# Performance work log

Hardware: AMD Instinct MI355X
Metric: run time of the kernel (lower is better)

## Reference

```python
import jax, jax.numpy as jnp
import numpy as np

GROUP_SIZE = 128

def setup_inputs() -> dict:
    key = jax.random.key(0)
    k0, k1, k2, k3 = jax.random.split(key, 4)
    B, S, K, N = 4, 16, 8192, 28672
    G = GROUP_SIZE
    x = jax.random.normal(k0, (B, S, K), dtype=jnp.float16)
    # packed uint8 stored as int32 (2 int4 nibbles per byte along K)
    w_packed = jax.random.randint(k1, (K // 2, N), 0, 256, dtype=jnp.int32)
    # per-group positive scales, typical magnitude for int4 quant of fp16 weights
    scales = (jax.random.uniform(k2, (K // G, N), dtype=jnp.float32) * 0.02 + 1e-4).astype(jnp.float16)
    bias = (jax.random.normal(k3, (N,), dtype=jnp.float16) * 0.02).astype(jnp.float16)
    return {"x": x, "w_packed": w_packed, "scales": scales, "bias": bias}

def _dequant(w_packed, scales):
    # w_packed: [K//2, N] ints in [0,256); low nibble -> even k, high nibble -> odd k
    low = (w_packed & 15) - 8          # [K//2, N] int32 in [-8, 7]
    high = ((w_packed >> 4) & 15) - 8  # [K//2, N]
    Kh, N = w_packed.shape
    w_int = jnp.stack([low, high], axis=1).reshape(Kh * 2, N)  # interleave -> [K, N]
    s = jnp.repeat(scales, GROUP_SIZE, axis=0)                 # [K, N] fp16
    return w_int.astype(jnp.float16) * s                       # [K, N] fp16

def reference(x, w_packed, scales, bias):
    # x: [B, S, K] fp16 -> y: [B, S, N] fp16
    w = _dequant(w_packed, scales)                 # [K, N] fp16
    lead = x.shape[:-1]
    x2 = x.reshape(-1, x.shape[-1])                # [M, K]
    # fp32 accumulation, fp16 output (matches Triton kernel's tl.dot accumulator)
    y = jnp.dot(x2, w, preferred_element_type=jnp.float32).astype(jnp.float16)
    y = y + bias
    return y.reshape(*lead, -1)
```

## Files before the change

### kernel.cpp

```cpp
#include <hip/hip_runtime.h>


typedef short  short8  __attribute__((ext_vector_type(8)));
typedef float  float4v __attribute__((ext_vector_type(4)));
typedef int    int4v   __attribute__((ext_vector_type(4)));
typedef unsigned int uint4v __attribute__((ext_vector_type(4)));

constexpr int Kd = 8192;
constexpr int Nd = 28672;
constexpr int KSPLIT = 4;

__device__ __forceinline__ unsigned f32_to_bf16_rn(float f) {
    unsigned u = __builtin_bit_cast(unsigned, f);
    return (u + 0x7FFFu + ((u >> 16) & 1u)) >> 16;
}

__device__ __forceinline__ void async16(const void* g, void* l) {
    __builtin_amdgcn_global_load_lds(
        (const __attribute__((address_space(1))) unsigned*)g,
        (__attribute__((address_space(3))) unsigned*)l, 16, 0, 0);
}

__global__ __launch_bounds__(256)
void init_y_kernel(const float* __restrict__ bias, float* __restrict__ y) {
    const int gid = blockIdx.x * 256 + threadIdx.x;
    const int m  = gid / (Nd / 4);
    const int nq = gid % (Nd / 4);
    ((float4v*)y)[(long)m * (Nd / 4) + nq] = ((const float4v*)bias)[nq];
}

__global__ __launch_bounds__(256)
void cvt_x_kernel(const float* __restrict__ x, unsigned short* __restrict__ o) {
    const int i = (blockIdx.x * 256 + threadIdx.x) * 8;
    float4v a = *(const float4v*)(x + i);
    float4v b = *(const float4v*)(x + i + 4);
    union { unsigned short s[8]; short8 v; } r;
    #pragma unroll
    for (int j = 0; j < 4; ++j) {
        r.s[j]     = (unsigned short)f32_to_bf16_rn(a[j]);
        r.s[4 + j] = (unsigned short)f32_to_bf16_rn(b[j]);
    }
    *(short8*)(o + i) = r.v;
}

__global__ __launch_bounds__(256, 3)
void int4_main_kernel(const unsigned short* __restrict__ xw,
                      const int*            __restrict__ wp,
                      const float*          __restrict__ scales,
                      float*                __restrict__ y)
{
    __shared__ unsigned wbA[2048], wbB[2048], wbC[2048];
    __shared__ unsigned xbA[2048], xbB[2048], xbC[2048];
    __shared__ unsigned sb[1024];

    const int t = threadIdx.x, lane = t & 63, wv = t >> 6;
    const int q = lane >> 4, c = lane & 15;
    const int l4 = lane >> 4, l15 = lane & 15;
    const int n0 = blockIdx.x * 64, kz = blockIdx.y;

    const int* wsrc0; const int* wsrc1;
    {
        int r0 = wv * 8 + 0 * 4 + l4, c0 = (l15 * 4) ^ (((wv * 2 + 0) & 3) << 4);
        int r1 = wv * 8 + 1 * 4 + l4, c1 = (l15 * 4) ^ (((wv * 2 + 1) & 3) << 4);
        wsrc0 = wp + (long)(kz * 1024 + r0) * Nd + n0 + c0;
        wsrc1 = wp + (long)(kz * 1024 + r1) * Nd + n0 + c1;
    }
    const unsigned short* xsrc0; const unsigned short* xsrc1;
    {
        int s0 = wv * 128 + 0 * 64 + lane, m0 = s0 >> 3, k0 = (s0 & 7) ^ (m0 & 7);
        int s1 = wv * 128 + 1 * 64 + lane, m1 = s1 >> 3, k1 = (s1 & 7) ^ (m1 & 7);
        xsrc0 = xw + (long)m0 * Kd + kz * 2048 + k0 * 8;
        xsrc1 = xw + (long)m1 * Kd + kz * 2048 + k1 * 8;
    }
    const int ldof = wv * 512;

    auto stage = [&](int hg, unsigned* wbuf, unsigned* xbuf) {
        const long wof = (long)hg * 32 * Nd;
        const long xof = (long)hg * 64;
        async16(wsrc0 + wof, wbuf + ldof);
        async16(wsrc1 + wof, wbuf + ldof + 256);
        async16(xsrc0 + xof, xbuf + ldof);
        async16(xsrc1 + xof, xbuf + ldof + 256);
    };

    {
        const float* ssrc = scales + (long)(kz * 16 + (t >> 4)) * Nd + n0 + (t & 15) * 4;
        async16(ssrc, sb + wv * 256);
    }
    stage(0, wbA, xbA);
    stage(1, wbB, xbB);

    float4v acc[4] = {};

    auto compute = [&](const unsigned* wbuf, const unsigned* xbuf, int g) {
        const float s   = __builtin_bit_cast(float, sb[g * 64 + wv * 16 + c]);
        const float m8s = -8.0f * s;
        #pragma unroll
        for (int it = 0; it < 2; ++it) {
            union { short8 h; unsigned u[4]; } bu;
            #pragma unroll
            for (int i = 0; i < 4; ++i) {
                unsigned v = wbuf[(it * 16 + q * 4 + i) * 64 + ((wv * 16 + c) ^ (q << 4))];
                float lo = fmaf((float)(v & 15u), s, m8s);
                float hi = fmaf((float)((v >> 4) & 15u), s, m8s);
                bu.u[i] = f32_to_bf16_rn(lo) | (f32_to_bf16_rn(hi) << 16);
            }
            __builtin_amdgcn_s_setprio(1);
            #pragma unroll
            for (int mt = 0; mt < 4; ++mt) {
                int m = mt * 16 + c;
                int slot = m * 8 + ((it * 4 + q) ^ (c & 7));
                short8 a = *(const short8*)(xbuf + slot * 4);
                acc[mt] = __builtin_amdgcn_mfma_f32_16x16x32_bf16(a, bu.h, acc[mt], 0, 0, 0);
            }
            __builtin_amdgcn_s_setprio(0);
        }
    };

    for (int g3 = 0; g3 < 10; ++g3) {
        const int ph = 3 * g3;
        stage(ph + 2, wbC, xbC);
        asm volatile("s_waitcnt vmcnt(8)\ns_barrier" ::: "memory");
        compute(wbA, xbA, ph >> 1);
        asm volatile("s_waitcnt lgkmcnt(0)\ns_barrier" ::: "memory");
        stage(ph + 3, wbA, xbA);
        asm volatile("s_waitcnt vmcnt(8)\ns_barrier" ::: "memory");
        compute(wbB, xbB, (ph + 1) >> 1);
        asm volatile("s_waitcnt lgkmcnt(0)\ns_barrier" ::: "memory");
        stage(ph + 4, wbB, xbB);
        asm volatile("s_waitcnt vmcnt(8)\ns_barrier" ::: "memory");
        compute(wbC, xbC, (ph + 2) >> 1);
        asm volatile("s_waitcnt lgkmcnt(0)\ns_barrier" ::: "memory");
    }
    asm volatile("s_waitcnt vmcnt(4)\ns_barrier" ::: "memory");
    compute(wbA, xbA, 15);
    asm volatile("s_waitcnt lgkmcnt(0)\ns_barrier" ::: "memory");
    asm volatile("s_waitcnt vmcnt(0)\ns_barrier" ::: "memory");
    compute(wbB, xbB, 15);

    const int nw = n0 + wv * 16 + c;
    #pragma unroll
    for (int mt = 0; mt < 4; ++mt)
        #pragma unroll
        for (int r = 0; r < 4; ++r)
            atomicAdd(&y[(long)(mt * 16 + q * 4 + r) * Nd + nw], acc[mt][r]);
}

__global__ __launch_bounds__(256, 6)
void int4_main_nows_kernel(const float* __restrict__ xf,
                           const int*   __restrict__ wp,
                           const float* __restrict__ scales,
                           float*       __restrict__ y)
{
    constexpr int LDS_STRIDE = 68;
    __shared__ unsigned lds_w[64 * LDS_STRIDE];
    const int t = threadIdx.x, lane = t & 63, wv = t >> 6;
    const int q = lane >> 4, c = lane & 15;
    const int n0 = blockIdx.x * 64, kz = blockIdx.y;
    const int sr = t >> 4, ss = t & 15;
    const int*   wp_b = wp + (long)(kz * 1024 + sr) * Nd + n0 + 4 * ss;
    const float* sc_b = scales + (long)(kz * 16) * Nd + n0 + 4 * ss;
    const float* xf_b = xf + (long)c * Kd + kz * 2048 + q * 8;
    float4v acc[4] = {};

    for (int g = 0; g < 16; ++g) {
        const float4v s4 = *(const float4v*)(sc_b + (long)g * Nd);
        const int* wg = wp_b + (long)g * 64 * Nd;
        #pragma unroll
        for (int i = 0; i < 4; ++i) {
            int4v v = *(const int4v*)(wg + (long)i * 16 * Nd);
            uint4v pk;
            #pragma unroll
            for (int j = 0; j < 4; ++j) {
                float lo = (float)((v[j] & 15) - 8) * s4[j];
                float hi = (float)(((v[j] >> 4) & 15) - 8) * s4[j];
                pk[j] = f32_to_bf16_rn(lo) | (f32_to_bf16_rn(hi) << 16);
            }
            *(uint4v*)&lds_w[(i * 16 + sr) * LDS_STRIDE + 4 * ss] = pk;
        }
        __syncthreads();
        const float* xg = xf_b + g * 128;
        #pragma unroll
        for (int it = 0; it < 4; ++it) {
            union { short8 h; unsigned u[4]; } bu;
            #pragma unroll
            for (int i = 0; i < 4; ++i)
                bu.u[i] = lds_w[(it * 16 + q * 4 + i) * LDS_STRIDE + wv * 16 + c];
            const short8 b = bu.h;
            const float* xk = xg + it * 32;
            #pragma unroll
            for (int mt = 0; mt < 4; ++mt) {
                float4v a0 = *(const float4v*)(xk + (long)mt * 16 * Kd);
                float4v a1 = *(const float4v*)(xk + (long)mt * 16 * Kd + 4);
                union { unsigned short s[8]; short8 v; } r;
                #pragma unroll
                for (int j = 0; j < 4; ++j) {
                    r.s[j]     = (unsigned short)f32_to_bf16_rn(a0[j]);
                    r.s[4 + j] = (unsigned short)f32_to_bf16_rn(a1[j]);
                }
                acc[mt] = __builtin_amdgcn_mfma_f32_16x16x32_bf16(r.v, b, acc[mt], 0, 0, 0);
            }
        }
        __syncthreads();
    }
    const int nw = n0 + wv * 16 + c;
    #pragma unroll
    for (int mt = 0; mt < 4; ++mt)
        #pragma unroll
        for (int r = 0; r < 4; ++r)
            atomicAdd(&y[(long)(mt * 16 + q * 4 + r) * Nd + nw], acc[mt][r]);
}

extern "C" void kernel_launch(void* const* d_in, const int* in_sizes, int n_in,
                              void* d_out, int out_size, void* d_ws, size_t ws_size,
                              hipStream_t stream) {
    const float* x      = (const float*)d_in[0];
    const int*   wp     = (const int*)d_in[1];
    const float* scales = (const float*)d_in[2];
    const float* bias   = (const float*)d_in[3];
    float*       y      = (float*)d_out;

    init_y_kernel<<<dim3(1792), dim3(256), 0, stream>>>(bias, y);

    const size_t xb_bytes = (size_t)64 * Kd * sizeof(unsigned short);
    dim3 grid(Nd / 64, KSPLIT);
    dim3 block(256);

    if (ws_size >= xb_bytes) {
        unsigned short* xb = (unsigned short*)d_ws;
        cvt_x_kernel<<<dim3(256), dim3(256), 0, stream>>>(x, xb);
        int4_main_kernel<<<grid, block, 0, stream>>>(xb, wp, scales, y);
    } else {
        int4_main_nows_kernel<<<grid, block, 0, stream>>>(x, wp, scales, y);
    }
}
```

Before: 627.2 us.

## Load packed int4 weights directly into registers instead of staging through LDS

Packed weight tiles now go from global memory straight into triple-buffered per-thread registers, with each lane loading the exact words it dequantizes. Activations and scales still stage through LDS. This drops the three weight LDS buffers, their LDS reads and bank traffic, and raises the launch-bounds occupancy hint from 3 to 4 blocks. The cost is more, narrower 4-byte global load instructions per stage, higher register use and retuned vmcnt waits that depend on the load issue order.

```diff
diff --git a/kernel.cpp b/kernel.cpp
--- a/kernel.cpp
+++ b/kernel.cpp
@@ -43,28 +43,21 @@
     *(short8*)(o + i) = r.v;
 }
 
-__global__ __launch_bounds__(256, 3)
+__global__ __launch_bounds__(256, 4)
 void int4_main_kernel(const unsigned short* __restrict__ xw,
                       const int*            __restrict__ wp,
                       const float*          __restrict__ scales,
                       float*                __restrict__ y)
 {
-    __shared__ unsigned wbA[2048], wbB[2048], wbC[2048];
     __shared__ unsigned xbA[2048], xbB[2048], xbC[2048];
     __shared__ unsigned sb[1024];
 
     const int t = threadIdx.x, lane = t & 63, wv = t >> 6;
     const int q = lane >> 4, c = lane & 15;
-    const int l4 = lane >> 4, l15 = lane & 15;
     const int n0 = blockIdx.x * 64, kz = blockIdx.y;
 
-    const int* wsrc0; const int* wsrc1;
-    {
-        int r0 = wv * 8 + 0 * 4 + l4, c0 = (l15 * 4) ^ (((wv * 2 + 0) & 3) << 4);
-        int r1 = wv * 8 + 1 * 4 + l4, c1 = (l15 * 4) ^ (((wv * 2 + 1) & 3) << 4);
-        wsrc0 = wp + (long)(kz * 1024 + r0) * Nd + n0 + c0;
-        wsrc1 = wp + (long)(kz * 1024 + r1) * Nd + n0 + c1;
-    }
+    const int* wbase = wp + (long)(kz * 1024 + q * 4) * Nd + n0 + wv * 16 + c;
+
     const unsigned short* xsrc0; const unsigned short* xsrc1;
     {
         int s0 = wv * 128 + 0 * 64 + lane, m0 = s0 >> 3, k0 = (s0 & 7) ^ (m0 & 7);
@@ -74,25 +67,23 @@
     }
     const int ldof = wv * 512;
 
-    auto stage = [&](int hg, unsigned* wbuf, unsigned* xbuf) {
-        const long wof = (long)hg * 32 * Nd;
+    auto stagex = [&](int hg, unsigned* xbuf) {
         const long xof = (long)hg * 64;
-        async16(wsrc0 + wof, wbuf + ldof);
-        async16(wsrc1 + wof, wbuf + ldof + 256);
         async16(xsrc0 + xof, xbuf + ldof);
         async16(xsrc1 + xof, xbuf + ldof + 256);
     };
-
-    {
-        const float* ssrc = scales + (long)(kz * 16 + (t >> 4)) * Nd + n0 + (t & 15) * 4;
-        async16(ssrc, sb + wv * 256);
-    }
-    stage(0, wbA, xbA);
-    stage(1, wbB, xbB);
+    auto loadw = [&](int ph, unsigned (&r)[8]) {
+        const int* b = wbase + (long)ph * 32 * Nd;
+        #pragma unroll
+        for (int it = 0; it < 2; ++it)
+            #pragma unroll
+            for (int i = 0; i < 4; ++i)
+                r[it * 4 + i] = (unsigned)b[(long)(it * 16 + i) * Nd];
+    };
 
     float4v acc[4] = {};
 
-    auto compute = [&](const unsigned* wbuf, const unsigned* xbuf, int g) {
+    auto compute = [&](const unsigned* xbuf, const unsigned (&wr)[8], int g) {
         const float s   = __builtin_bit_cast(float, sb[g * 64 + wv * 16 + c]);
         const float m8s = -8.0f * s;
         #pragma unroll
@@ -100,7 +91,7 @@
             union { short8 h; unsigned u[4]; } bu;
             #pragma unroll
             for (int i = 0; i < 4; ++i) {
-                unsigned v = wbuf[(it * 16 + q * 4 + i) * 64 + ((wv * 16 + c) ^ (q << 4))];
+                unsigned v = wr[it * 4 + i];
                 float lo = fmaf((float)(v & 15u), s, m8s);
                 float hi = fmaf((float)((v >> 4) & 15u), s, m8s);
                 bu.u[i] = f32_to_bf16_rn(lo) | (f32_to_bf16_rn(hi) << 16);
@@ -117,26 +108,49 @@
         }
     };
 
+    unsigned wr0[8], wr1[8], wr2[8];
+
+    {
+        const float* ssrc = scales + (long)(kz * 16 + (t >> 4)) * Nd + n0 + (t & 15) * 4;
+        async16(ssrc, sb + wv * 256);
+    }
+    stagex(0, xbA);
+    __builtin_amdgcn_sched_barrier(0);
+    loadw(0, wr0);
+    __builtin_amdgcn_sched_barrier(0);
+    stagex(1, xbB);
+    __builtin_amdgcn_sched_barrier(0);
+    loadw(1, wr1);
+    __builtin_amdgcn_sched_barrier(0);
+
     for (int g3 = 0; g3 < 10; ++g3) {
-        const int ph = 3 * g3;
-        stage(ph + 2, wbC, xbC);
-        asm volatile("s_waitcnt vmcnt(8)\ns_barrier" ::: "memory");
-        compute(wbA, xbA, ph >> 1);
+        const int p = 3 * g3;
+        stagex(p + 2, xbC);
+        __builtin_amdgcn_sched_barrier(0);
+        loadw(p + 2, wr2);
+        asm volatile("s_waitcnt vmcnt(28)\ns_barrier" ::: "memory");
+        compute(xbA, wr0, p >> 1);
         asm volatile("s_waitcnt lgkmcnt(0)\ns_barrier" ::: "memory");
-        stage(ph + 3, wbA, xbA);
-        asm volatile("s_waitcnt vmcnt(8)\ns_barrier" ::: "memory");
-        compute(wbB, xbB, (ph + 1) >> 1);
+
+        stagex(p + 3, xbA);
+        __builtin_amdgcn_sched_barrier(0);
+        loadw(p + 3, wr0);
+        asm volatile("s_waitcnt vmcnt(28)\ns_barrier" ::: "memory");
+        compute(xbB, wr1, (p + 1) >> 1);
         asm volatile("s_waitcnt lgkmcnt(0)\ns_barrier" ::: "memory");
-        stage(ph + 4, wbB, xbB);
-        asm volatile("s_waitcnt vmcnt(8)\ns_barrier" ::: "memory");
-        compute(wbC, xbC, (ph + 2) >> 1);
+
+        stagex(p + 4, xbB);
+        __builtin_amdgcn_sched_barrier(0);
+        loadw(p + 4, wr1);
+        asm volatile("s_waitcnt vmcnt(28)\ns_barrier" ::: "memory");
+        compute(xbC, wr2, (p + 2) >> 1);
         asm volatile("s_waitcnt lgkmcnt(0)\ns_barrier" ::: "memory");
     }
-    asm volatile("s_waitcnt vmcnt(4)\ns_barrier" ::: "memory");
-    compute(wbA, xbA, 15);
+    asm volatile("s_waitcnt vmcnt(18)\ns_barrier" ::: "memory");
+    compute(xbA, wr0, 15);
     asm volatile("s_waitcnt lgkmcnt(0)\ns_barrier" ::: "memory");
-    asm volatile("s_waitcnt vmcnt(0)\ns_barrier" ::: "memory");
-    compute(wbB, xbB, 15);
+    asm volatile("s_waitcnt vmcnt(8)\ns_barrier" ::: "memory");
+    compute(xbB, wr1, 15);
 
     const int nw = n0 + wv * 16 + c;
     #pragma unroll
```

Measured after the change: 634.6 us. No clear change (+1.2%).
